# Kernel tuning notes

Hardware: AMD Instinct MI355X
Metric: run time of the kernel (lower is better)

## Reference

```python
import jax, jax.numpy as jnp
import numpy as np

EMBED_DIM = 128
N_EMBED = 10000
INPUT_SHAPE = (8, 64, 32, EMBED_DIM)


def setup_inputs() -> dict:
    key = jax.random.key(0)
    k1, k2 = jax.random.split(key)
    inputs = jax.random.normal(k1, INPUT_SHAPE, dtype=jnp.float32)
    cluster_mean = jax.random.normal(k2, (EMBED_DIM, N_EMBED), dtype=jnp.float32)
    return {"inputs": inputs, "cluster_mean": cluster_mean}


def reference(inputs, cluster_mean):
    embed_dim = cluster_mean.shape[0]
    # Flatten all leading dims: (N, D)
    samples = inputs.reshape(-1, embed_dim)
    # Squared euclidean distance to each code: (N, n_embed)
    dist = (
        jnp.sum(samples ** 2, axis=1, keepdims=True)
        - 2.0 * samples @ cluster_mean
        + jnp.sum(cluster_mean ** 2, axis=0, keepdims=True)
    )
    cluster_index = jnp.argmin(dist, axis=1).reshape(inputs.shape[:-1])
    # Embedding lookup from transposed codebook: (..., D)
    quantize = cluster_mean.T[cluster_index]
    q_loss = jnp.mean((quantize - jax.lax.stop_gradient(inputs)) ** 2)
    e_loss = jnp.mean((jax.lax.stop_gradient(quantize) - inputs) ** 2)
    loss = q_loss + 0.25 * e_loss
    # Straight-through estimator
    outputs = inputs + jax.lax.stop_gradient(quantize - inputs)
    return outputs, loss
```

## Files before the change

kernel.cpp:

```cpp
#include <hip/hip_runtime.h>

#define EMBED 128
#define NCODE 10000
#define NSAMP 16384
#define NCODE_PAD 10240
#define NSPLIT 8
#define SPLIT_CODES 1280
#define NCHUNK 20
#define CHUNK_ELEMS 8192
#define OUT_ELEMS (NSAMP * EMBED)
#define TAU 0.002f
#define NSEG 16

typedef float f32x16 __attribute__((ext_vector_type(16)));
typedef short s16x8 __attribute__((ext_vector_type(8)));
typedef unsigned short ushort_t;
typedef unsigned long long u64;

#define OFF_AH  0
#define OFF_AL  2621440
#define OFF_CT  5242880
#define OFF_CN  10485760
#define OFF_KEY 10526720
#define OFF_C2  11575296
#define OFF_IDX 12099584
#define OFF_RL  12165120
#define OFF_CNT 12230656
#define OFF_BEST 12230720

__device__ __forceinline__ unsigned short f2bf(float f) {
    unsigned u = __float_as_uint(f);
    return (unsigned short)((u + 0x7fffu + ((u >> 16) & 1u)) >> 16);
}
__device__ __forceinline__ float bf2f(unsigned short h) {
    return __uint_as_float(((unsigned)h) << 16);
}
__device__ __forceinline__ unsigned ordf(float f) {
    unsigned u = __float_as_uint(f);
    return (u & 0x80000000u) ? ~u : (u | 0x80000000u);
}
__device__ __forceinline__ float unordf(unsigned o) {
    return __uint_as_float((o & 0x80000000u) ? (o ^ 0x80000000u) : ~o);
}

__global__ __launch_bounds__(256) void prep_norm(const float* __restrict__ C,
                                                 float* __restrict__ cnorm,
                                                 float* __restrict__ out,
                                                 int* __restrict__ counter) {
    int j = blockIdx.x * 256 + threadIdx.x;
    if (j == 0) { out[OUT_ELEMS] = 0.f; *counter = 0; }
    if (j >= NCODE_PAD) return;
    if (j >= NCODE) { cnorm[j] = 3.0e38f; return; }
    float s = 0.f;
#pragma unroll 8
    for (int d = 0; d < EMBED; ++d) {
        float v = C[d * NCODE + j];
        s = fmaf(v, v, s);
    }
    cnorm[j] = s;
}

__global__ __launch_bounds__(256) void prep_c4(const float* __restrict__ C,
                                               ushort_t* __restrict__ Ah,
                                               ushort_t* __restrict__ Al,
                                               float* __restrict__ CT) {
    int o = blockIdx.x * 256 + threadIdx.x;
    int n  = o % NCODE_PAD;
    int kg = o / NCODE_PAD;
    int split = n / SPLIT_CODES;
    int rem   = n % SPLIT_CODES;
    int chunk = rem >> 6;
    int mb    = (rem >> 5) & 1;
    int row   = rem & 31;
    int ks = kg >> 1, kh = kg & 1;
    size_t eoff = (size_t)(split * NCHUNK + chunk) * CHUNK_ELEMS
                + (size_t)(mb * 4096 + (ks * 2 + kh) * 256 + row * 8);
    int k0 = kg * 8;
    float f[8];
#pragma unroll
    for (int j = 0; j < 8; ++j)
        f[j] = (n < NCODE) ? C[(size_t)(k0 + j) * NCODE + n] : 0.f;
    *(float4*)(CT + (size_t)n * EMBED + k0)     = make_float4(f[0], f[1], f[2], f[3]);
    *(float4*)(CT + (size_t)n * EMBED + k0 + 4) = make_float4(f[4], f[5], f[6], f[7]);
    s16x8 vh, vl;
#pragma unroll
    for (int j = 0; j < 8; ++j) {
        unsigned short h = f2bf(f[j]);
        vh[j] = (short)h;
        vl[j] = (short)f2bf(f[j] - bf2f(h));
    }
    *(s16x8*)(Ah + eoff) = vh;
    *(s16x8*)(Al + eoff) = vl;
}

__global__ __launch_bounds__(512, 2) void vq7(const float* __restrict__ X,
                                              const ushort_t* __restrict__ Ah,
                                              const ushort_t* __restrict__ Al,
                                              const float* __restrict__ cnorm,
                                              u64* __restrict__ candKey,
                                              unsigned* __restrict__ cand2) {
    __shared__ ushort_t Bs[3 * 2 * CHUNK_ELEMS];
    __shared__ float cns[SPLIT_CODES];
    const int t    = threadIdx.x;
    const int lane = t & 63;
    const int wave = t >> 6;
    const int ln   = lane & 31;
    const int kh   = lane >> 5;
    const int split = blockIdx.y;
    const int m0    = blockIdx.x * 512;
    const int sbase = split * SPLIT_CODES;

    s16x8 bh[2][8], bl[2][8];
#pragma unroll
    for (int g = 0; g < 2; ++g) {
        int m = m0 + wave * 64 + g * 32 + ln;
#pragma unroll
        for (int ks = 0; ks < 8; ++ks) {
            const float* src = X + (size_t)m * EMBED + ks * 16 + kh * 8;
            float4 f0 = *(const float4*)src;
            float4 f1 = *(const float4*)(src + 4);
            float f[8] = {f0.x, f0.y, f0.z, f0.w, f1.x, f1.y, f1.z, f1.w};
            s16x8 vh, vl;
#pragma unroll
            for (int j = 0; j < 8; ++j) {
                float v = -2.f * f[j];
                unsigned short h = f2bf(v);
                vh[j] = (short)h;
                vl[j] = (short)f2bf(v - bf2f(h));
            }
            bh[g][ks] = vh;
            bl[g][ks] = vl;
        }
    }

    for (int i = t; i < SPLIT_CODES; i += 512) cns[i] = cnorm[sbase + i];

    float v1[2] = {3.4e38f, 3.4e38f}, v2[2] = {3.4e38f, 3.4e38f};
    int   j1[2] = {0, 0};

    auto ldsw = (__attribute__((address_space(3))) ushort_t*)Bs;
    const int woff = wave * 1024;
    const size_t chbase = (size_t)(split * NCHUNK) * CHUNK_ELEMS;

    auto stage = [&](int cc, int buf) {
        const size_t sb = chbase + (size_t)cc * CHUNK_ELEMS;
        const ushort_t* sh = Ah + sb + woff + lane * 8;
        const ushort_t* sl = Al + sb + woff + lane * 8;
        const int db = buf * 2 * CHUNK_ELEMS + woff;
#pragma unroll
        for (int i = 0; i < 2; ++i) {
            __builtin_amdgcn_global_load_lds(
                (const __attribute__((address_space(1))) void*)(sh + i * 512),
                (__attribute__((address_space(3))) void*)(ldsw + db + i * 512),
                16, 0, 0);
            __builtin_amdgcn_global_load_lds(
                (const __attribute__((address_space(1))) void*)(sl + i * 512),
                (__attribute__((address_space(3))) void*)(ldsw + db + CHUNK_ELEMS + i * 512),
                16, 0, 0);
        }
    };

    stage(0, 0);
    stage(1, 1);
    __syncthreads();

    int b = 0;
    for (int c = 0; c < NCHUNK; ++c) {
        if (c + 2 < NCHUNK) {
            int nb = b + 2; if (nb >= 3) nb -= 3;
            stage(c + 2, nb);
        }

        const int bb = b * 2 * CHUNK_ELEMS;
        const int cb = c * 64 + 4 * kh;

#pragma unroll
        for (int mb = 0; mb < 2; ++mb) {
            f32x16 acc0 = {0,0,0,0,0,0,0,0,0,0,0,0,0,0,0,0};
            f32x16 acc1 = {0,0,0,0,0,0,0,0,0,0,0,0,0,0,0,0};
            __builtin_amdgcn_s_setprio(1);
#pragma unroll
            for (int ks = 0; ks < 8; ++ks) {
                const int fo = bb + mb * 4096 + (ks * 2 + kh) * 256 + ln * 8;
                s16x8 a_h = *(const s16x8*)&Bs[fo];
                s16x8 a_l = *(const s16x8*)&Bs[CHUNK_ELEMS + fo];
                acc0 = __builtin_amdgcn_mfma_f32_32x32x16_bf16(a_h, bh[0][ks], acc0, 0, 0, 0);
                acc1 = __builtin_amdgcn_mfma_f32_32x32x16_bf16(a_h, bh[1][ks], acc1, 0, 0, 0);
                acc0 = __builtin_amdgcn_mfma_f32_32x32x16_bf16(a_h, bl[0][ks], acc0, 0, 0, 0);
                acc1 = __builtin_amdgcn_mfma_f32_32x32x16_bf16(a_h, bl[1][ks], acc1, 0, 0, 0);
                acc0 = __builtin_amdgcn_mfma_f32_32x32x16_bf16(a_l, bh[0][ks], acc0, 0, 0, 0);
                acc1 = __builtin_amdgcn_mfma_f32_32x32x16_bf16(a_l, bh[1][ks], acc1, 0, 0, 0);
            }
            __builtin_amdgcn_s_setprio(0);
#pragma unroll
            for (int r = 0; r < 16; ++r) {
                const int cc = cb + mb * 32 + ((r & 3) + 8 * (r >> 2));
                const float cn = cns[cc];
                const int code = sbase + cc;
                float d;
                d = acc0[r] + cn;
                if (d < v1[0]) { v2[0] = v1[0]; v1[0] = d; j1[0] = code; }
                else           { v2[0] = fminf(v2[0], d); }
                d = acc1[r] + cn;
                if (d < v1[1]) { v2[1] = v1[1]; v1[1] = d; j1[1] = code; }
                else           { v2[1] = fminf(v2[1], d); }
            }
        }

        if (c < NCHUNK - 2) asm volatile("s_waitcnt vmcnt(4)" ::: "memory");
        else                asm volatile("s_waitcnt vmcnt(0)" ::: "memory");
        asm volatile("s_barrier" ::: "memory");
        ++b; if (b >= 3) b = 0;
    }

#pragma unroll
    for (int g = 0; g < 2; ++g) {
        float ov1 = __shfl_xor(v1[g], 32, 64);
        int   oj1 = __shfl_xor(j1[g], 32, 64);
        float ov2 = __shfl_xor(v2[g], 32, 64);
        float hi = fmaxf(v1[g], ov1);
        v2[g] = fminf(fminf(v2[g], ov2), hi);
        if (ov1 < v1[g] || (ov1 == v1[g] && oj1 < j1[g])) { v1[g] = ov1; j1[g] = oj1; }
        if (kh == 0) {
            int m = m0 + wave * 64 + g * 32 + ln;
            candKey[(size_t)m * NSPLIT + split] =
                ((u64)ordf(v1[g]) << 32) | (unsigned)j1[g];
            cand2[(size_t)m * NSPLIT + split] = ordf(v2[g]);
        }
    }
}

__global__ __launch_bounds__(256) void outfin_k(const float* __restrict__ X,
                                                const float* __restrict__ CT,
                                                const u64* __restrict__ candKey,
                                                const unsigned* __restrict__ cand2,
                                                int* __restrict__ idxf,
                                                int* __restrict__ rlist,
                                                int* __restrict__ counter,
                                                u64* __restrict__ wsBest,
                                                float* __restrict__ out) {
    __shared__ float red[4];
    const int t = threadIdx.x;
    const int m = blockIdx.x * 8 + (t >> 5);
    const int l = t & 31;

    int code = 0;
    if (l == 0) {
        u64 best = 0xffffffffffffffffull;
        float v2 = 3.4e38f;
#pragma unroll
        for (int s = 0; s < NSPLIT; ++s) {
            u64 k = candKey[(size_t)m * NSPLIT + s];
            unsigned o2 = cand2[(size_t)m * NSPLIT + s];
            if (k < best) {
                if (best != 0xffffffffffffffffull)
                    v2 = fminf(v2, unordf((unsigned)(best >> 32)));
                best = k;
                v2 = fminf(v2, unordf(o2));
            } else {
                v2 = fminf(v2, unordf((unsigned)(k >> 32)));
            }
        }
        code = (int)(unsigned)(best & 0xffffffffu);
        idxf[m] = code;
        float v1 = unordf((unsigned)(best >> 32));
        if (v2 - v1 <= TAU) {
            rlist[atomicAdd(counter, 1)] = m;
            wsBest[m] = 0xffffffffffffffffull;
        }
    }
    code = __shfl(code, 0, 32);

    float4 q = *(const float4*)(CT + (size_t)code * EMBED + l * 4);
    float4 x = *(const float4*)(X + (size_t)m * EMBED + l * 4);
    *(float4*)(out + (size_t)m * EMBED + l * 4) = q;
    float dx = q.x - x.x, dy = q.y - x.y, dz = q.z - x.z, dw = q.w - x.w;
    float lsum = dx * dx + dy * dy + dz * dz + dw * dw;
#pragma unroll
    for (int off = 1; off < 64; off <<= 1) lsum += __shfl_xor(lsum, off, 64);
    if ((t & 63) == 0) red[t >> 6] = lsum;
    __syncthreads();
    if (t == 0)
        atomicAdd(out + OUT_ELEMS,
                  (red[0] + red[1] + red[2] + red[3]) * (1.25f / (float)OUT_ELEMS));
}

__global__ __launch_bounds__(256) void rescue_seg(const float* __restrict__ X,
                                                  const float* __restrict__ CT,
                                                  const float* __restrict__ cnorm,
                                                  const int* __restrict__ rlist,
                                                  const int* __restrict__ counter,
                                                  u64* __restrict__ wsBest) {
    __shared__ float xs[EMBED];
    __shared__ u64 wk[4];
    const int t = threadIdx.x;
    const int lane = t & 63;
    const int wave = t >> 6;
    const int hw = t & 31;
    const int slot = t >> 5;
    const int cnt = *counter;
    const int nw = cnt * NSEG;

    for (int w = blockIdx.x; w < nw; w += gridDim.x) {
        const int s = w >> 4, seg = w & 15;
        const int m = rlist[s];
        __syncthreads();
        if (t < 32) {
            float4 v = *(const float4*)(X + (size_t)m * EMBED + t * 4);
            xs[t * 4 + 0] = v.x; xs[t * 4 + 1] = v.y;
            xs[t * 4 + 2] = v.z; xs[t * 4 + 3] = v.w;
        }
        __syncthreads();
        const float x0 = xs[hw * 4 + 0], x1 = xs[hw * 4 + 1];
        const float x2 = xs[hw * 4 + 2], x3 = xs[hw * 4 + 3];
        const int base = seg * 625;
        const int jend = base + 625;
        u64 bk = 0xffffffffffffffffull;
        for (int it = 0; it < 20; ++it) {
            const int r0 = base + it * 32 + slot * 4;
            float4 c0, c1, c2, c3;
            bool ok0 = (r0 + 0 < jend), ok1 = (r0 + 1 < jend);
            bool ok2 = (r0 + 2 < jend), ok3 = (r0 + 3 < jend);
            c0 = ok0 ? *(const float4*)(CT + (size_t)(r0 + 0) * EMBED + hw * 4) : make_float4(0, 0, 0, 0);
            c1 = ok1 ? *(const float4*)(CT + (size_t)(r0 + 1) * EMBED + hw * 4) : make_float4(0, 0, 0, 0);
            c2 = ok2 ? *(const float4*)(CT + (size_t)(r0 + 2) * EMBED + hw * 4) : make_float4(0, 0, 0, 0);
            c3 = ok3 ? *(const float4*)(CT + (size_t)(r0 + 3) * EMBED + hw * 4) : make_float4(0, 0, 0, 0);
            float p0 = x0 * c0.x, p1 = x0 * c1.x, p2 = x0 * c2.x, p3 = x0 * c3.x;
            p0 = fmaf(x1, c0.y, p0); p1 = fmaf(x1, c1.y, p1);
            p2 = fmaf(x1, c2.y, p2); p3 = fmaf(x1, c3.y, p3);
            p0 = fmaf(x2, c0.z, p0); p1 = fmaf(x2, c1.z, p1);
            p2 = fmaf(x2, c2.z, p2); p3 = fmaf(x2, c3.z, p3);
            p0 = fmaf(x3, c0.w, p0); p1 = fmaf(x3, c1.w, p1);
            p2 = fmaf(x3, c2.w, p2); p3 = fmaf(x3, c3.w, p3);
#pragma unroll
            for (int off = 1; off < 32; off <<= 1) {
                p0 += __shfl_xor(p0, off, 32);
                p1 += __shfl_xor(p1, off, 32);
                p2 += __shfl_xor(p2, off, 32);
                p3 += __shfl_xor(p3, off, 32);
            }
            if (hw == 0) {
                if (ok0) { u64 k = ((u64)ordf(fmaf(-2.f, p0, cnorm[r0 + 0])) << 32) | (unsigned)(r0 + 0); if (k < bk) bk = k; }
                if (ok1) { u64 k = ((u64)ordf(fmaf(-2.f, p1, cnorm[r0 + 1])) << 32) | (unsigned)(r0 + 1); if (k < bk) bk = k; }
                if (ok2) { u64 k = ((u64)ordf(fmaf(-2.f, p2, cnorm[r0 + 2])) << 32) | (unsigned)(r0 + 2); if (k < bk) bk = k; }
                if (ok3) { u64 k = ((u64)ordf(fmaf(-2.f, p3, cnorm[r0 + 3])) << 32) | (unsigned)(r0 + 3); if (k < bk) bk = k; }
            }
        }
#pragma unroll
        for (int off = 1; off < 64; off <<= 1) {
            u64 o = __shfl_xor(bk, off, 64);
            if (o < bk) bk = o;
        }
        if (lane == 0) wk[wave] = bk;
        __syncthreads();
        if (t == 0) {
            u64 b = wk[0];
            if (wk[1] < b) b = wk[1];
            if (wk[2] < b) b = wk[2];
            if (wk[3] < b) b = wk[3];
            atomicMin(&wsBest[m], b);
        }
    }
}

__global__ __launch_bounds__(256) void patch_k(const float* __restrict__ X,
                                               const float* __restrict__ CT,
                                               const int* __restrict__ rlist,
                                               const int* __restrict__ counter,
                                               const u64* __restrict__ wsBest,
                                               const int* __restrict__ idxf,
                                               float* __restrict__ out) {
    const int t = threadIdx.x;
    const int l = t & 31, sl = t >> 5;
    const int cnt = *counter;
    for (int s = blockIdx.x * 8 + sl; s < cnt; s += gridDim.x * 8) {
        int m = rlist[s];
        u64 key = wsBest[m];
        int jn = (int)(unsigned)(key & 0xffffffffu);
        int jo = idxf[m];
        if (jn == jo) continue;
        float4 qn = *(const float4*)(CT + (size_t)jn * EMBED + l * 4);
        float4 qo = *(const float4*)(CT + (size_t)jo * EMBED + l * 4);
        float4 x  = *(const float4*)(X + (size_t)m * EMBED + l * 4);
        *(float4*)(out + (size_t)m * EMBED + l * 4) = qn;
        float dn = (qn.x - x.x) * (qn.x - x.x) + (qn.y - x.y) * (qn.y - x.y)
                 + (qn.z - x.z) * (qn.z - x.z) + (qn.w - x.w) * (qn.w - x.w);
        float dp = (qo.x - x.x) * (qo.x - x.x) + (qo.y - x.y) * (qo.y - x.y)
                 + (qo.z - x.z) * (qo.z - x.z) + (qo.w - x.w) * (qo.w - x.w);
        float delta = dn - dp;
#pragma unroll
        for (int off = 1; off < 32; off <<= 1) delta += __shfl_xor(delta, off, 32);
        if (l == 0)
            atomicAdd(out + OUT_ELEMS, delta * (1.25f / (float)OUT_ELEMS));
    }
}

extern "C" void kernel_launch(void* const* d_in, const int* in_sizes, int n_in,
                              void* d_out, int out_size, void* d_ws, size_t ws_size,
                              hipStream_t stream) {
    const float* X = (const float*)d_in[0];
    const float* C = (const float*)d_in[1];
    float* out = (float*)d_out;
    char* ws = (char*)d_ws;

    ushort_t* Ah = (ushort_t*)(ws + OFF_AH);
    ushort_t* Al = (ushort_t*)(ws + OFF_AL);
    float* CT    = (float*)(ws + OFF_CT);
    float* cnorm = (float*)(ws + OFF_CN);
    u64* candKey = (u64*)(ws + OFF_KEY);
    unsigned* cand2 = (unsigned*)(ws + OFF_C2);
    int* idxf    = (int*)(ws + OFF_IDX);
    int* rlist   = (int*)(ws + OFF_RL);
    int* counter = (int*)(ws + OFF_CNT);
    u64* wsBest  = (u64*)(ws + OFF_BEST);

    prep_norm<<<NCODE_PAD / 256, 256, 0, stream>>>(C, cnorm, out, counter);
    prep_c4<<<(NCODE_PAD * 16) / 256, 256, 0, stream>>>(C, Ah, Al, CT);
    vq7<<<dim3(NSAMP / 512, NSPLIT), 512, 0, stream>>>(X, Ah, Al, cnorm, candKey, cand2);
    outfin_k<<<NSAMP / 8, 256, 0, stream>>>(X, CT, candKey, cand2, idxf, rlist, counter, wsBest, out);
    rescue_seg<<<1024, 256, 0, stream>>>(X, CT, cnorm, rlist, counter, wsBest);
    patch_k<<<64, 256, 0, stream>>>(X, CT, rlist, counter, wsBest, idxf, out);
}
```

Baseline: 258.1 us.

## Software-pipeline MFMA and argmin epilogue with smaller blocks and double buffering

Shrinks the distance kernel's blocks from 512 to 256 threads (more blocks) and moves from triple to double buffering of codebook chunks in LDS, with each wave staging twice as many loads. The argmin epilogue for one 32-code half is now interleaved with the MFMA phase of the next half, so VALU compare work can overlap matrix work. The top-2 update is rewritten branch-free using fmin/fmax. This trades the deeper prefetch and the explicit vmcnt waits for full __syncthreads, and holds more accumulator registers live, which may raise register pressure.

```diff
diff --git a/kernel.cpp b/kernel.cpp
--- a/kernel.cpp
+++ b/kernel.cpp
@@ -93,13 +93,13 @@
     *(s16x8*)(Al + eoff) = vl;
 }
 
-__global__ __launch_bounds__(512, 2) void vq7(const float* __restrict__ X,
+__global__ __launch_bounds__(256, 2) void vq7(const float* __restrict__ X,
                                               const ushort_t* __restrict__ Ah,
                                               const ushort_t* __restrict__ Al,
                                               const float* __restrict__ cnorm,
                                               u64* __restrict__ candKey,
                                               unsigned* __restrict__ cand2) {
-    __shared__ ushort_t Bs[3 * 2 * CHUNK_ELEMS];
+    __shared__ ushort_t Bs[2 * 2 * CHUNK_ELEMS];
     __shared__ float cns[SPLIT_CODES];
     const int t    = threadIdx.x;
     const int lane = t & 63;
@@ -107,7 +107,7 @@
     const int ln   = lane & 31;
     const int kh   = lane >> 5;
     const int split = blockIdx.y;
-    const int m0    = blockIdx.x * 512;
+    const int m0    = blockIdx.x * 256;
     const int sbase = split * SPLIT_CODES;
 
     s16x8 bh[2][8], bl[2][8];
@@ -133,13 +133,13 @@
         }
     }
 
-    for (int i = t; i < SPLIT_CODES; i += 512) cns[i] = cnorm[sbase + i];
+    for (int i = t; i < SPLIT_CODES; i += 256) cns[i] = cnorm[sbase + i];
 
     float v1[2] = {3.4e38f, 3.4e38f}, v2[2] = {3.4e38f, 3.4e38f};
     int   j1[2] = {0, 0};
 
     auto ldsw = (__attribute__((address_space(3))) ushort_t*)Bs;
-    const int woff = wave * 1024;
+    const int woff = wave * 2048;
     const size_t chbase = (size_t)(split * NCHUNK) * CHUNK_ELEMS;
 
     auto stage = [&](int cc, int buf) {
@@ -148,7 +148,7 @@
         const ushort_t* sl = Al + sb + woff + lane * 8;
         const int db = buf * 2 * CHUNK_ELEMS + woff;
 #pragma unroll
-        for (int i = 0; i < 2; ++i) {
+        for (int i = 0; i < 4; ++i) {
             __builtin_amdgcn_global_load_lds(
                 (const __attribute__((address_space(1))) void*)(sh + i * 512),
                 (__attribute__((address_space(3))) void*)(ldsw + db + i * 512),
@@ -160,58 +160,73 @@
         }
     };
 
+#define MFMA_PHASE(BB, MB, P0, P1)                                            \
+    {                                                                         \
+        P0 = (f32x16){0,0,0,0,0,0,0,0,0,0,0,0,0,0,0,0};                       \
+        P1 = (f32x16){0,0,0,0,0,0,0,0,0,0,0,0,0,0,0,0};                       \
+        _Pragma("unroll")                                                     \
+        for (int ks = 0; ks < 8; ++ks) {                                      \
+            const int fo = (BB) + (MB) * 4096 + (ks * 2 + kh) * 256 + ln * 8; \
+            s16x8 a_h = *(const s16x8*)&Bs[fo];                               \
+            s16x8 a_l = *(const s16x8*)&Bs[CHUNK_ELEMS + fo];                 \
+            P0 = __builtin_amdgcn_mfma_f32_32x32x16_bf16(a_h, bh[0][ks], P0, 0, 0, 0); \
+            P1 = __builtin_amdgcn_mfma_f32_32x32x16_bf16(a_h, bh[1][ks], P1, 0, 0, 0); \
+            P0 = __builtin_amdgcn_mfma_f32_32x32x16_bf16(a_h, bl[0][ks], P0, 0, 0, 0); \
+            P1 = __builtin_amdgcn_mfma_f32_32x32x16_bf16(a_h, bl[1][ks], P1, 0, 0, 0); \
+            P0 = __builtin_amdgcn_mfma_f32_32x32x16_bf16(a_l, bh[0][ks], P0, 0, 0, 0); \
+            P1 = __builtin_amdgcn_mfma_f32_32x32x16_bf16(a_l, bh[1][ks], P1, 0, 0, 0); \
+        }                                                                     \
+    }
+
+#define EPI(P0, P1, CB)                                                       \
+    {                                                                         \
+        _Pragma("unroll")                                                     \
+        for (int r = 0; r < 16; ++r) {                                        \
+            const int cc = (CB) + ((r & 3) + 8 * (r >> 2));                   \
+            const float cn = cns[cc];                                         \
+            const int code = sbase + cc;                                      \
+            float d0 = P0[r] + cn;                                            \
+            v2[0] = fminf(v2[0], fmaxf(d0, v1[0]));                           \
+            if (d0 < v1[0]) j1[0] = code;                                     \
+            v1[0] = fminf(v1[0], d0);                                         \
+            float d1 = P1[r] + cn;                                            \
+            v2[1] = fminf(v2[1], fmaxf(d1, v1[1]));                           \
+            if (d1 < v1[1]) j1[1] = code;                                     \
+            v1[1] = fminf(v1[1], d1);                                         \
+        }                                                                     \
+    }
+
+    f32x16 aA0, aA1, aB0, aB1;
+    int cbA, cbB;
+
     stage(0, 0);
-    stage(1, 1);
     __syncthreads();
-
-    int b = 0;
-    for (int c = 0; c < NCHUNK; ++c) {
-        if (c + 2 < NCHUNK) {
-            int nb = b + 2; if (nb >= 3) nb -= 3;
-            stage(c + 2, nb);
-        }
-
+    {
+        stage(1, 1);
+        const int cb = 4 * kh;
+        MFMA_PHASE(0, 0, aA0, aA1);
+        cbA = cb;
+        MFMA_PHASE(0, 1, aB0, aB1);
+        EPI(aA0, aA1, cbA);
+        cbB = cb + 32;
+        __syncthreads();
+    }
+
+    for (int c = 1; c < NCHUNK; ++c) {
+        const int b = c & 1;
+        if (c + 1 < NCHUNK) stage(c + 1, 1 - b);
         const int bb = b * 2 * CHUNK_ELEMS;
         const int cb = c * 64 + 4 * kh;
 
-#pragma unroll
-        for (int mb = 0; mb < 2; ++mb) {
-            f32x16 acc0 = {0,0,0,0,0,0,0,0,0,0,0,0,0,0,0,0};
-            f32x16 acc1 = {0,0,0,0,0,0,0,0,0,0,0,0,0,0,0,0};
-            __builtin_amdgcn_s_setprio(1);
-#pragma unroll
-            for (int ks = 0; ks < 8; ++ks) {
-                const int fo = bb + mb * 4096 + (ks * 2 + kh) * 256 + ln * 8;
-                s16x8 a_h = *(const s16x8*)&Bs[fo];
-                s16x8 a_l = *(const s16x8*)&Bs[CHUNK_ELEMS + fo];
-                acc0 = __builtin_amdgcn_mfma_f32_32x32x16_bf16(a_h, bh[0][ks], acc0, 0, 0, 0);
-                acc1 = __builtin_amdgcn_mfma_f32_32x32x16_bf16(a_h, bh[1][ks], acc1, 0, 0, 0);
-                acc0 = __builtin_amdgcn_mfma_f32_32x32x16_bf16(a_h, bl[0][ks], acc0, 0, 0, 0);
-                acc1 = __builtin_amdgcn_mfma_f32_32x32x16_bf16(a_h, bl[1][ks], acc1, 0, 0, 0);
-                acc0 = __builtin_amdgcn_mfma_f32_32x32x16_bf16(a_l, bh[0][ks], acc0, 0, 0, 0);
-                acc1 = __builtin_amdgcn_mfma_f32_32x32x16_bf16(a_l, bh[1][ks], acc1, 0, 0, 0);
-            }
-            __builtin_amdgcn_s_setprio(0);
-#pragma unroll
-            for (int r = 0; r < 16; ++r) {
-                const int cc = cb + mb * 32 + ((r & 3) + 8 * (r >> 2));
-                const float cn = cns[cc];
-                const int code = sbase + cc;
-                float d;
-                d = acc0[r] + cn;
-                if (d < v1[0]) { v2[0] = v1[0]; v1[0] = d; j1[0] = code; }
-                else           { v2[0] = fminf(v2[0], d); }
-                d = acc1[r] + cn;
-                if (d < v1[1]) { v2[1] = v1[1]; v1[1] = d; j1[1] = code; }
-                else           { v2[1] = fminf(v2[1], d); }
-            }
-        }
-
-        if (c < NCHUNK - 2) asm volatile("s_waitcnt vmcnt(4)" ::: "memory");
-        else                asm volatile("s_waitcnt vmcnt(0)" ::: "memory");
-        asm volatile("s_barrier" ::: "memory");
-        ++b; if (b >= 3) b = 0;
-    }
+        MFMA_PHASE(bb, 0, aA0, aA1);
+        EPI(aB0, aB1, cbB);
+        cbA = cb;
+        MFMA_PHASE(bb, 1, aB0, aB1);
+        EPI(aA0, aA1, cbA);
+        cbB = cb + 32;
+        __syncthreads();
+    }
+    EPI(aB0, aB1, cbB);
 
 #pragma unroll
     for (int g = 0; g < 2; ++g) {
@@ -228,6 +243,8 @@
             cand2[(size_t)m * NSPLIT + split] = ordf(v2[g]);
         }
     }
+#undef MFMA_PHASE
+#undef EPI
 }
 
 __global__ __launch_bounds__(256) void outfin_k(const float* __restrict__ X,
@@ -416,7 +433,7 @@
 
     prep_norm<<<NCODE_PAD / 256, 256, 0, stream>>>(C, cnorm, out, counter);
     prep_c4<<<(NCODE_PAD * 16) / 256, 256, 0, stream>>>(C, Ah, Al, CT);
-    vq7<<<dim3(NSAMP / 512, NSPLIT), 512, 0, stream>>>(X, Ah, Al, cnorm, candKey, cand2);
+    vq7<<<dim3(NSAMP / 256, NSPLIT), 256, 0, stream>>>(X, Ah, Al, cnorm, candKey, cand2);
     outfin_k<<<NSAMP / 8, 256, 0, stream>>>(X, CT, candKey, cand2, idxf, rlist, counter, wsBest, out);
     rescue_seg<<<1024, 256, 0, stream>>>(X, CT, cnorm, rlist, counter, wsBest);
     patch_k<<<64, 256, 0, stream>>>(X, CT, rlist, counter, wsBest, idxf, out);
```

Measured after the change: 253.0 us. -2.0%, faster.

## Halve per-wave samples in VQ kernel for higher occupancy, double-buffer LDS

Applied to the files above, without the earlier changes.

The main distance kernel now gives each wave one 32-sample group instead of two. This halves the MFMA accumulator and B-fragment registers, and launch bounds are raised to allow four blocks per CU. LDS staging drops from triple to double buffering with a plain __syncthreads per chunk, and the k-loop splits into two independent accumulator chains to expose more MFMA parallelism. The argmin update becomes branchless, and prep_norm splits the 128-dim reduction across four thread groups. In exchange, each staged codebook chunk serves half as many samples, doubling global/L2 traffic for the codebook and the grid size, and the prefetch distance is shorter.

```diff
diff --git a/kernel.cpp b/kernel.cpp
--- a/kernel.cpp
+++ b/kernel.cpp
@@ -47,17 +47,27 @@
                                                  float* __restrict__ cnorm,
                                                  float* __restrict__ out,
                                                  int* __restrict__ counter) {
-    int j = blockIdx.x * 256 + threadIdx.x;
-    if (j == 0) { out[OUT_ELEMS] = 0.f; *counter = 0; }
-    if (j >= NCODE_PAD) return;
-    if (j >= NCODE) { cnorm[j] = 3.0e38f; return; }
+    __shared__ float red[256];
+    const int t  = threadIdx.x;
+    const int jl = t & 63;
+    const int dh = t >> 6;
+    const int j  = blockIdx.x * 64 + jl;
+    if (blockIdx.x == 0 && t == 0) { out[OUT_ELEMS] = 0.f; *counter = 0; }
     float s = 0.f;
+    if (j < NCODE) {
 #pragma unroll 8
-    for (int d = 0; d < EMBED; ++d) {
-        float v = C[d * NCODE + j];
-        s = fmaf(v, v, s);
-    }
-    cnorm[j] = s;
+        for (int d = dh * 32; d < dh * 32 + 32; ++d) {
+            float v = C[d * NCODE + j];
+            s = fmaf(v, v, s);
+        }
+    }
+    red[t] = s;
+    __syncthreads();
+    if (t < 64) {
+        float v = red[t] + red[t + 64] + red[t + 128] + red[t + 192];
+        int jj = blockIdx.x * 64 + t;
+        cnorm[jj] = (jj < NCODE) ? v : 3.0e38f;
+    }
 }
 
 __global__ __launch_bounds__(256) void prep_c4(const float* __restrict__ C,
@@ -93,13 +103,13 @@
     *(s16x8*)(Al + eoff) = vl;
 }
 
-__global__ __launch_bounds__(512, 2) void vq7(const float* __restrict__ X,
+__global__ __launch_bounds__(512, 4) void vq7(const float* __restrict__ X,
                                               const ushort_t* __restrict__ Ah,
                                               const ushort_t* __restrict__ Al,
                                               const float* __restrict__ cnorm,
                                               u64* __restrict__ candKey,
                                               unsigned* __restrict__ cand2) {
-    __shared__ ushort_t Bs[3 * 2 * CHUNK_ELEMS];
+    __shared__ ushort_t Bs[2 * 2 * CHUNK_ELEMS];
     __shared__ float cns[SPLIT_CODES];
     const int t    = threadIdx.x;
     const int lane = t & 63;
@@ -107,13 +117,12 @@
     const int ln   = lane & 31;
     const int kh   = lane >> 5;
     const int split = blockIdx.y;
-    const int m0    = blockIdx.x * 512;
+    const int m0    = blockIdx.x * 256;
     const int sbase = split * SPLIT_CODES;
 
-    s16x8 bh[2][8], bl[2][8];
-#pragma unroll
-    for (int g = 0; g < 2; ++g) {
-        int m = m0 + wave * 64 + g * 32 + ln;
+    s16x8 bh[8], bl[8];
+    {
+        const int m = m0 + wave * 32 + ln;
 #pragma unroll
         for (int ks = 0; ks < 8; ++ks) {
             const float* src = X + (size_t)m * EMBED + ks * 16 + kh * 8;
@@ -128,15 +137,15 @@
                 vh[j] = (short)h;
                 vl[j] = (short)f2bf(v - bf2f(h));
             }
-            bh[g][ks] = vh;
-            bl[g][ks] = vl;
+            bh[ks] = vh;
+            bl[ks] = vl;
         }
     }
 
     for (int i = t; i < SPLIT_CODES; i += 512) cns[i] = cnorm[sbase + i];
 
-    float v1[2] = {3.4e38f, 3.4e38f}, v2[2] = {3.4e38f, 3.4e38f};
-    int   j1[2] = {0, 0};
+    float v1 = 3.4e38f, v2 = 3.4e38f;
+    int   j1 = 0;
 
     auto ldsw = (__attribute__((address_space(3))) ushort_t*)Bs;
     const int woff = wave * 1024;
@@ -161,71 +170,59 @@
     };
 
     stage(0, 0);
-    stage(1, 1);
     __syncthreads();
 
-    int b = 0;
     for (int c = 0; c < NCHUNK; ++c) {
-        if (c + 2 < NCHUNK) {
-            int nb = b + 2; if (nb >= 3) nb -= 3;
-            stage(c + 2, nb);
-        }
-
+        const int b = c & 1;
+        if (c + 1 < NCHUNK) stage(c + 1, 1 - b);
         const int bb = b * 2 * CHUNK_ELEMS;
         const int cb = c * 64 + 4 * kh;
 
 #pragma unroll
         for (int mb = 0; mb < 2; ++mb) {
-            f32x16 acc0 = {0,0,0,0,0,0,0,0,0,0,0,0,0,0,0,0};
-            f32x16 acc1 = {0,0,0,0,0,0,0,0,0,0,0,0,0,0,0,0};
-            __builtin_amdgcn_s_setprio(1);
-#pragma unroll
-            for (int ks = 0; ks < 8; ++ks) {
-                const int fo = bb + mb * 4096 + (ks * 2 + kh) * 256 + ln * 8;
-                s16x8 a_h = *(const s16x8*)&Bs[fo];
-                s16x8 a_l = *(const s16x8*)&Bs[CHUNK_ELEMS + fo];
-                acc0 = __builtin_amdgcn_mfma_f32_32x32x16_bf16(a_h, bh[0][ks], acc0, 0, 0, 0);
-                acc1 = __builtin_amdgcn_mfma_f32_32x32x16_bf16(a_h, bh[1][ks], acc1, 0, 0, 0);
-                acc0 = __builtin_amdgcn_mfma_f32_32x32x16_bf16(a_h, bl[0][ks], acc0, 0, 0, 0);
-                acc1 = __builtin_amdgcn_mfma_f32_32x32x16_bf16(a_h, bl[1][ks], acc1, 0, 0, 0);
-                acc0 = __builtin_amdgcn_mfma_f32_32x32x16_bf16(a_l, bh[0][ks], acc0, 0, 0, 0);
-                acc1 = __builtin_amdgcn_mfma_f32_32x32x16_bf16(a_l, bh[1][ks], acc1, 0, 0, 0);
-            }
-            __builtin_amdgcn_s_setprio(0);
+            f32x16 aE = {0,0,0,0,0,0,0,0,0,0,0,0,0,0,0,0};
+            f32x16 aO = {0,0,0,0,0,0,0,0,0,0,0,0,0,0,0,0};
+#pragma unroll
+            for (int kp = 0; kp < 4; ++kp) {
+                const int k0 = 2 * kp, k1 = 2 * kp + 1;
+                const int f0 = bb + mb * 4096 + (k0 * 2 + kh) * 256 + ln * 8;
+                const int f1 = bb + mb * 4096 + (k1 * 2 + kh) * 256 + ln * 8;
+                s16x8 h0 = *(const s16x8*)&Bs[f0];
+                s16x8 l0 = *(const s16x8*)&Bs[CHUNK_ELEMS + f0];
+                s16x8 h1 = *(const s16x8*)&Bs[f1];
+                s16x8 l1 = *(const s16x8*)&Bs[CHUNK_ELEMS + f1];
+                aE = __builtin_amdgcn_mfma_f32_32x32x16_bf16(h0, bh[k0], aE, 0, 0, 0);
+                aO = __builtin_amdgcn_mfma_f32_32x32x16_bf16(h1, bh[k1], aO, 0, 0, 0);
+                aE = __builtin_amdgcn_mfma_f32_32x32x16_bf16(h0, bl[k0], aE, 0, 0, 0);
+                aO = __builtin_amdgcn_mfma_f32_32x32x16_bf16(h1, bl[k1], aO, 0, 0, 0);
+                aE = __builtin_amdgcn_mfma_f32_32x32x16_bf16(l0, bh[k0], aE, 0, 0, 0);
+                aO = __builtin_amdgcn_mfma_f32_32x32x16_bf16(l1, bh[k1], aO, 0, 0, 0);
+            }
+            const int cb2 = cb + mb * 32;
 #pragma unroll
             for (int r = 0; r < 16; ++r) {
-                const int cc = cb + mb * 32 + ((r & 3) + 8 * (r >> 2));
-                const float cn = cns[cc];
-                const int code = sbase + cc;
-                float d;
-                d = acc0[r] + cn;
-                if (d < v1[0]) { v2[0] = v1[0]; v1[0] = d; j1[0] = code; }
-                else           { v2[0] = fminf(v2[0], d); }
-                d = acc1[r] + cn;
-                if (d < v1[1]) { v2[1] = v1[1]; v1[1] = d; j1[1] = code; }
-                else           { v2[1] = fminf(v2[1], d); }
-            }
-        }
-
-        if (c < NCHUNK - 2) asm volatile("s_waitcnt vmcnt(4)" ::: "memory");
-        else                asm volatile("s_waitcnt vmcnt(0)" ::: "memory");
-        asm volatile("s_barrier" ::: "memory");
-        ++b; if (b >= 3) b = 0;
-    }
-
-#pragma unroll
-    for (int g = 0; g < 2; ++g) {
-        float ov1 = __shfl_xor(v1[g], 32, 64);
-        int   oj1 = __shfl_xor(j1[g], 32, 64);
-        float ov2 = __shfl_xor(v2[g], 32, 64);
-        float hi = fmaxf(v1[g], ov1);
-        v2[g] = fminf(fminf(v2[g], ov2), hi);
-        if (ov1 < v1[g] || (ov1 == v1[g] && oj1 < j1[g])) { v1[g] = ov1; j1[g] = oj1; }
+                const int cc = cb2 + ((r & 3) + 8 * (r >> 2));
+                const float d = aE[r] + aO[r] + cns[cc];
+                v2 = fminf(v2, fmaxf(d, v1));
+                if (d < v1) j1 = sbase + cc;
+                v1 = fminf(v1, d);
+            }
+        }
+        __syncthreads();
+    }
+
+    {
+        float ov1 = __shfl_xor(v1, 32, 64);
+        int   oj1 = __shfl_xor(j1, 32, 64);
+        float ov2 = __shfl_xor(v2, 32, 64);
+        float hi = fmaxf(v1, ov1);
+        v2 = fminf(fminf(v2, ov2), hi);
+        if (ov1 < v1 || (ov1 == v1 && oj1 < j1)) { v1 = ov1; j1 = oj1; }
         if (kh == 0) {
-            int m = m0 + wave * 64 + g * 32 + ln;
+            int m = m0 + wave * 32 + ln;
             candKey[(size_t)m * NSPLIT + split] =
-                ((u64)ordf(v1[g]) << 32) | (unsigned)j1[g];
-            cand2[(size_t)m * NSPLIT + split] = ordf(v2[g]);
+                ((u64)ordf(v1) << 32) | (unsigned)j1;
+            cand2[(size_t)m * NSPLIT + split] = ordf(v2);
         }
     }
 }
@@ -414,9 +411,9 @@
     int* counter = (int*)(ws + OFF_CNT);
     u64* wsBest  = (u64*)(ws + OFF_BEST);
 
-    prep_norm<<<NCODE_PAD / 256, 256, 0, stream>>>(C, cnorm, out, counter);
+    prep_norm<<<NCODE_PAD / 64, 256, 0, stream>>>(C, cnorm, out, counter);
     prep_c4<<<(NCODE_PAD * 16) / 256, 256, 0, stream>>>(C, Ah, Al, CT);
-    vq7<<<dim3(NSAMP / 512, NSPLIT), 512, 0, stream>>>(X, Ah, Al, cnorm, candKey, cand2);
+    vq7<<<dim3(NSAMP / 256, NSPLIT), 512, 0, stream>>>(X, Ah, Al, cnorm, candKey, cand2);
     outfin_k<<<NSAMP / 8, 256, 0, stream>>>(X, CT, candKey, cand2, idxf, rlist, counter, wsBest, out);
     rescue_seg<<<1024, 256, 0, stream>>>(X, CT, cnorm, rlist, counter, wsBest);
     patch_k<<<64, 256, 0, stream>>>(X, CT, rlist, counter, wsBest, idxf, out);
```

Result: no change. 261.0 us (+1.1%).
